# Optimization experiments

Hardware: AMD Instinct MI355X
Metric: run time of the kernel (lower is better)

Reference implementation:

```python
import jax, jax.numpy as jnp
import numpy as np

B, L, D, I = 64, 196, 2048, 512

def setup_inputs() -> dict:
    key = jax.random.key(0)
    ks = jax.random.split(key, 8)
    s_f = 1.0 / np.sqrt(D)
    s_h = 1.0 / np.sqrt(I)
    s_a = 1.0 / np.sqrt(I)
    return {
        "feature_vectors": jax.random.normal(ks[0], (B, L, D), dtype=jnp.float32),
        "hidden_state": jax.random.normal(ks[1], (B, I), dtype=jnp.float32),
        "W_f": jax.random.uniform(ks[2], (D, I), jnp.float32, -s_f, s_f),
        "b_f": jax.random.uniform(ks[3], (I,), jnp.float32, -s_f, s_f),
        "W_h": jax.random.uniform(ks[4], (I, I), jnp.float32, -s_h, s_h),
        "b_h": jax.random.uniform(ks[5], (I,), jnp.float32, -s_h, s_h),
        "W_a": jax.random.uniform(ks[6], (I, D), jnp.float32, -s_a, s_a),
        "b_a": jax.random.uniform(ks[7], (D,), jnp.float32, -s_a, s_a),
    }

def reference(feature_vectors, hidden_state, W_f, b_f, W_h, b_h, W_a, b_a):
    # fv: [B,L,D], hidden: [B,I]
    fv_shaped = jnp.einsum('bld,di->bli', feature_vectors, W_f) + b_f      # [B,L,I]
    hs_shaped = hidden_state @ W_h + b_h                                   # [B,I]
    e = jnp.einsum('bli,id->bld', fv_shaped + hs_shaped[:, None, :], W_a) + b_a  # [B,L,D]
    alpha = jax.nn.softmax(e, axis=1)                                      # softmax over L locations
    z = jnp.sum(alpha * feature_vectors, axis=1)                           # [B,D] (vectorized loop)
    return (z, alpha)
```

## Files before the change

### kernel.cpp

```cpp
#include <hip/hip_runtime.h>

#define B_ 64
#define L_ 196
#define D_ 2048
#define I_ 512
#define M_ (B_*L_)

typedef __attribute__((ext_vector_type(8))) short bf16x8;
typedef __attribute__((ext_vector_type(4))) float f32x4;
typedef unsigned short u16;

__device__ __forceinline__ u16 f2bf(float x){
  unsigned u = __float_as_uint(x);
  u += 0x7fffu + ((u >> 16) & 1u);
  return (u16)(u >> 16);
}

__device__ __forceinline__ void gld16(const void* g, void* l){
  __builtin_amdgcn_global_load_lds(
      (const __attribute__((address_space(1))) void*)g,
      (__attribute__((address_space(3))) void*)l, 16, 0, 0);
}

__global__ void cvt_bf16_kernel(const float* __restrict__ in, u16* __restrict__ out, int n4){
  int i = blockIdx.x*blockDim.x + threadIdx.x;
  int stride = gridDim.x*blockDim.x;
  for (; i < n4; i += stride){
    float4 v = ((const float4*)in)[i];
    ushort4 o;
    o.x = f2bf(v.x); o.y = f2bf(v.y); o.z = f2bf(v.z); o.w = f2bf(v.w);
    ((ushort4*)out)[i] = o;
  }
}

__global__ void transpose_cvt_kernel(const float* __restrict__ in, u16* __restrict__ out, int R, int C){
  __shared__ float tile[32][33];
  int c0 = blockIdx.x*32, r0 = blockIdx.y*32;
  int tx = threadIdx.x, ty = threadIdx.y;
  for (int i=0;i<32;i+=8)
    tile[ty+i][tx] = in[(size_t)(r0+ty+i)*C + c0 + tx];
  __syncthreads();
  for (int i=0;i<32;i+=8)
    out[(size_t)(c0+ty+i)*R + r0 + tx] = f2bf(tile[tx][ty+i]);
}

__global__ void hs_kernel(const float* __restrict__ hidden, const float* __restrict__ Wh,
                          const float* __restrict__ bh, float* __restrict__ hs){
  int n = blockIdx.x*blockDim.x + threadIdx.x;
  int b = blockIdx.y;
  const float* hrow = hidden + b*I_;
  float a0=0.f,a1=0.f,a2=0.f,a3=0.f;
  for (int k=0;k<I_;k+=4){
    a0 = fmaf(hrow[k+0], Wh[(size_t)(k+0)*I_ + n], a0);
    a1 = fmaf(hrow[k+1], Wh[(size_t)(k+1)*I_ + n], a1);
    a2 = fmaf(hrow[k+2], Wh[(size_t)(k+2)*I_ + n], a2);
    a3 = fmaf(hrow[k+3], Wh[(size_t)(k+3)*I_ + n], a3);
  }
  hs[b*I_ + n] = bh[n] + ((a0+a1)+(a2+a3));
}

__launch_bounds__(256)
__global__ void gemm128_kernel(const u16* __restrict__ A,
                               const u16* __restrict__ Bt,
                               int K, int N, int mode,
                               const float* __restrict__ bias,
                               const float* __restrict__ hs,
                               u16* __restrict__ outb,
                               float* __restrict__ outf)
{
  __shared__ __align__(16) u16 Als[128*32];
  __shared__ __align__(16) u16 Bls[128*32];

  const int tid  = threadIdx.x;
  const int lane = tid & 63;
  const int wave = tid >> 6;
  const int m0 = blockIdx.y * 128;
  const int n0 = blockIdx.x * 128;

  const int wrow = (wave & 1) * 64;
  const int wcol = (wave >> 1) * 64;
  const int q  = lane >> 4;
  const int mr = lane & 15;

  const int j0 = wave * 2;
  const int r0i = j0*16     + (lane>>2);
  const int r1i = (j0+1)*16 + (lane>>2);
  const int kc0 = (lane&3) ^ ((r0i>>2)&3);
  const int kc1 = (lane&3) ^ ((r1i>>2)&3);
  const u16* Ag0 = A  + (size_t)(m0 + r0i)*K + kc0*8;
  const u16* Ag1 = A  + (size_t)(m0 + r1i)*K + kc1*8;
  const u16* Bg0 = Bt + (size_t)(n0 + r0i)*K + kc0*8;
  const u16* Bg1 = Bt + (size_t)(n0 + r1i)*K + kc1*8;
  u16* Al0 = Als + (size_t)j0*512;
  u16* Al1 = Als + (size_t)(j0+1)*512;
  u16* Bl0 = Bls + (size_t)j0*512;
  u16* Bl1 = Bls + (size_t)(j0+1)*512;

  int aoff[4], boff[4];
  #pragma unroll
  for (int t=0;t<4;t++){
    int R = wrow + t*16 + mr;
    aoff[t] = (R*4 + (q ^ ((R>>2)&3)))*8;
    int C = wcol + t*16 + mr;
    boff[t] = (C*4 + (q ^ ((C>>2)&3)))*8;
  }

  f32x4 acc[4][4];
  #pragma unroll
  for (int i=0;i<4;i++)
    #pragma unroll
    for (int j=0;j<4;j++) acc[i][j] = (f32x4){0.f,0.f,0.f,0.f};

  for (int k0 = 0; k0 < K; k0 += 32){
    __syncthreads();
    gld16(Ag0 + k0, Al0);
    gld16(Ag1 + k0, Al1);
    gld16(Bg0 + k0, Bl0);
    gld16(Bg1 + k0, Bl1);
    __syncthreads();
    bf16x8 af[4], bg[4];
    #pragma unroll
    for (int t=0;t<4;t++){
      af[t] = *(const bf16x8*)(Als + aoff[t]);
      bg[t] = *(const bf16x8*)(Bls + boff[t]);
    }
    #pragma unroll
    for (int i=0;i<4;i++)
      #pragma unroll
      for (int j=0;j<4;j++)
        acc[i][j] = __builtin_amdgcn_mfma_f32_16x16x32_bf16(af[i], bg[j], acc[i][j], 0,0,0);
  }

  #pragma unroll
  for (int i=0;i<4;i++){
    #pragma unroll
    for (int j=0;j<4;j++){
      int gcol = n0 + wcol + j*16 + mr;
      float bcol = bias[gcol];
      #pragma unroll
      for (int r=0;r<4;r++){
        int grow = m0 + wrow + i*16 + q*4 + r;
        float v = acc[i][j][r] + bcol;
        if (mode == 0){
          int batch = grow / L_;
          outb[(size_t)grow*N + gcol] = f2bf(v + hs[batch*I_ + gcol]);
        } else {
          outf[(size_t)grow*N + gcol] = v;
        }
      }
    }
  }
}

__global__ void softmax_z_kernel(const float* __restrict__ fv, float* __restrict__ out){
  int d = blockIdx.x*blockDim.x + threadIdx.x;
  int b = blockIdx.y;
  float* e = out + (size_t)B_*D_ + (size_t)b*L_*D_ + d;
  const float* f = fv + (size_t)b*L_*D_ + d;
  float m = -3.4e38f, s = 0.f;
  for (int l=0;l<L_;++l){
    float x = e[(size_t)l*D_];
    float nm = fmaxf(m, x);
    s = s*__expf(m-nm) + __expf(x-nm);
    m = nm;
  }
  float inv = 1.f/s;
  float z = 0.f;
  for (int l=0;l<L_;++l){
    float x = e[(size_t)l*D_];
    float a = __expf(x-m)*inv;
    e[(size_t)l*D_] = a;
    z = fmaf(a, f[(size_t)l*D_], z);
  }
  out[(size_t)b*D_ + d] = z;
}

extern "C" void kernel_launch(void* const* d_in, const int* in_sizes, int n_in,
                              void* d_out, int out_size, void* d_ws, size_t ws_size,
                              hipStream_t stream){
  (void)in_sizes; (void)n_in; (void)out_size; (void)ws_size;
  const float* fv     = (const float*)d_in[0];
  const float* hidden = (const float*)d_in[1];
  const float* W_f    = (const float*)d_in[2];
  const float* b_f    = (const float*)d_in[3];
  const float* W_h    = (const float*)d_in[4];
  const float* b_h    = (const float*)d_in[5];
  const float* W_a    = (const float*)d_in[6];
  const float* b_a    = (const float*)d_in[7];
  float* out = (float*)d_out;

  char* ws = (char*)d_ws;
  u16*   fv_bf = (u16*)ws;
  u16*   t_bf  = (u16*)(ws + 51380224);
  u16*   WfT   = (u16*)(ws + 64225280);
  u16*   WaT   = (u16*)(ws + 66322432);
  float* hsbuf = (float*)(ws + 68419584);

  cvt_bf16_kernel<<<4096, 256, 0, stream>>>(fv, fv_bf, (B_*L_*D_)/4);
  transpose_cvt_kernel<<<dim3(I_/32, D_/32), dim3(32,8), 0, stream>>>(W_f, WfT, D_, I_);
  transpose_cvt_kernel<<<dim3(D_/32, I_/32), dim3(32,8), 0, stream>>>(W_a, WaT, I_, D_);
  hs_kernel<<<dim3(I_/256, B_), 256, 0, stream>>>(hidden, W_h, b_h, hsbuf);

  gemm128_kernel<<<dim3(I_/128, M_/128), 256, 0, stream>>>(fv_bf, WfT, D_, I_, 0, b_f, hsbuf, t_bf, nullptr);
  gemm128_kernel<<<dim3(D_/128, M_/128), 256, 0, stream>>>(t_bf, WaT, I_, D_, 1, b_a, nullptr, nullptr, out + B_*D_);

  softmax_z_kernel<<<dim3(D_/256, B_), 256, 0, stream>>>(fv, out);
}
```

Before: 389.8 us.

## Template GEMM with BK=64 tiles, narrower first GEMM, and parallel softmax over L

The GEMM becomes a template with compile-time K, N and mode and a K tile of 64 instead of 32, which halves the number of barrier pairs per K. The first GEMM uses 128x64 tiles so it launches twice as many blocks for the small N=512. The softmax kernel splits the 196 locations across four waves and keeps values in registers, so e is read once instead of twice and more blocks run; the cost is shared-memory reductions and a higher register count.

```diff
diff --git a/kernel.cpp b/kernel.cpp
--- a/kernel.cpp
+++ b/kernel.cpp
@@ -59,120 +59,148 @@
   hs[b*I_ + n] = bh[n] + ((a0+a1)+(a2+a3));
 }
 
+template<int BN, int K, int MODE, int NLD>
 __launch_bounds__(256)
-__global__ void gemm128_kernel(const u16* __restrict__ A,
-                               const u16* __restrict__ Bt,
-                               int K, int N, int mode,
-                               const float* __restrict__ bias,
-                               const float* __restrict__ hs,
-                               u16* __restrict__ outb,
-                               float* __restrict__ outf)
+__global__ void gemm_kernel(const u16* __restrict__ A, const u16* __restrict__ Bt,
+                            const float* __restrict__ bias, const float* __restrict__ hs,
+                            u16* __restrict__ outb, float* __restrict__ outf)
 {
-  __shared__ __align__(16) u16 Als[128*32];
-  __shared__ __align__(16) u16 Bls[128*32];
-
-  const int tid  = threadIdx.x;
-  const int lane = tid & 63;
-  const int wave = tid >> 6;
-  const int m0 = blockIdx.y * 128;
-  const int n0 = blockIdx.x * 128;
-
+  constexpr int BM = 128, BK = 64;
+  constexpr int NF = BN/32;
+  constexpr int AW = 4;
+  constexpr int BW = BN/32;
+
+  __shared__ __align__(16) u16 Als[BM*BK];
+  __shared__ __align__(16) u16 Bls[BN*BK];
+
+  const int tid = threadIdx.x, lane = tid & 63, wave = tid >> 6;
+  const int m0 = blockIdx.y * BM, n0 = blockIdx.x * BN;
+  const int q = lane >> 4, mr = lane & 15;
   const int wrow = (wave & 1) * 64;
-  const int wcol = (wave >> 1) * 64;
-  const int q  = lane >> 4;
-  const int mr = lane & 15;
-
-  const int j0 = wave * 2;
-  const int r0i = j0*16     + (lane>>2);
-  const int r1i = (j0+1)*16 + (lane>>2);
-  const int kc0 = (lane&3) ^ ((r0i>>2)&3);
-  const int kc1 = (lane&3) ^ ((r1i>>2)&3);
-  const u16* Ag0 = A  + (size_t)(m0 + r0i)*K + kc0*8;
-  const u16* Ag1 = A  + (size_t)(m0 + r1i)*K + kc1*8;
-  const u16* Bg0 = Bt + (size_t)(n0 + r0i)*K + kc0*8;
-  const u16* Bg1 = Bt + (size_t)(n0 + r1i)*K + kc1*8;
-  u16* Al0 = Als + (size_t)j0*512;
-  u16* Al1 = Als + (size_t)(j0+1)*512;
-  u16* Bl0 = Bls + (size_t)j0*512;
-  u16* Bl1 = Bls + (size_t)(j0+1)*512;
-
-  int aoff[4], boff[4];
-  #pragma unroll
-  for (int t=0;t<4;t++){
-    int R = wrow + t*16 + mr;
-    aoff[t] = (R*4 + (q ^ ((R>>2)&3)))*8;
-    int C = wcol + t*16 + mr;
-    boff[t] = (C*4 + (q ^ ((C>>2)&3)))*8;
-  }
-
-  f32x4 acc[4][4];
+  const int wcol = (wave >> 1) * (BN/2);
+
+  const int lrow = lane >> 3;
+  const int kc   = (lane & 7) ^ lrow;
+
+  const u16* Ag[AW]; u16* Al[AW];
+  #pragma unroll
+  for (int u=0; u<AW; ++u){
+    int j = wave*AW + u;
+    Ag[u] = A + (size_t)(m0 + j*8 + lrow)*K + kc*8;
+    Al[u] = Als + j*512;
+  }
+  const u16* Bg[BW]; u16* Bl[BW];
+  #pragma unroll
+  for (int u=0; u<BW; ++u){
+    int j = wave*BW + u;
+    Bg[u] = Bt + (size_t)(n0 + j*8 + lrow)*K + kc*8;
+    Bl[u] = Bls + j*512;
+  }
+
+  int aoff[4][2], boff[NF][2];
   #pragma unroll
   for (int i=0;i<4;i++)
     #pragma unroll
-    for (int j=0;j<4;j++) acc[i][j] = (f32x4){0.f,0.f,0.f,0.f};
-
-  for (int k0 = 0; k0 < K; k0 += 32){
+    for (int s=0;s<2;s++){
+      int R = wrow + i*16 + mr;
+      aoff[i][s] = R*64 + (((s*4+q) ^ (mr&7))*8);
+    }
+  #pragma unroll
+  for (int j=0;j<NF;j++)
+    #pragma unroll
+    for (int s=0;s<2;s++){
+      int C = wcol + j*16 + mr;
+      boff[j][s] = C*64 + (((s*4+q) ^ (mr&7))*8);
+    }
+
+  f32x4 acc[4][NF];
+  #pragma unroll
+  for (int i=0;i<4;i++)
+    #pragma unroll
+    for (int j=0;j<NF;j++) acc[i][j] = (f32x4){0.f,0.f,0.f,0.f};
+
+  for (int k0=0; k0<K; k0+=BK){
     __syncthreads();
-    gld16(Ag0 + k0, Al0);
-    gld16(Ag1 + k0, Al1);
-    gld16(Bg0 + k0, Bl0);
-    gld16(Bg1 + k0, Bl1);
+    #pragma unroll
+    for (int u=0;u<AW;++u) gld16(Ag[u] + k0, Al[u]);
+    #pragma unroll
+    for (int u=0;u<BW;++u) gld16(Bg[u] + k0, Bl[u]);
     __syncthreads();
-    bf16x8 af[4], bg[4];
-    #pragma unroll
-    for (int t=0;t<4;t++){
-      af[t] = *(const bf16x8*)(Als + aoff[t]);
-      bg[t] = *(const bf16x8*)(Bls + boff[t]);
-    }
-    #pragma unroll
-    for (int i=0;i<4;i++)
-      #pragma unroll
-      for (int j=0;j<4;j++)
-        acc[i][j] = __builtin_amdgcn_mfma_f32_16x16x32_bf16(af[i], bg[j], acc[i][j], 0,0,0);
+    #pragma unroll
+    for (int s=0;s<2;s++){
+      bf16x8 af[4], bg[NF];
+      #pragma unroll
+      for (int i=0;i<4;i++) af[i] = *(const bf16x8*)(Als + aoff[i][s]);
+      #pragma unroll
+      for (int j=0;j<NF;j++) bg[j] = *(const bf16x8*)(Bls + boff[j][s]);
+      #pragma unroll
+      for (int i=0;i<4;i++)
+        #pragma unroll
+        for (int j=0;j<NF;j++)
+          acc[i][j] = __builtin_amdgcn_mfma_f32_16x16x32_bf16(af[i], bg[j], acc[i][j], 0,0,0);
+    }
   }
 
   #pragma unroll
   for (int i=0;i<4;i++){
     #pragma unroll
-    for (int j=0;j<4;j++){
+    for (int j=0;j<NF;j++){
       int gcol = n0 + wcol + j*16 + mr;
       float bcol = bias[gcol];
       #pragma unroll
       for (int r=0;r<4;r++){
         int grow = m0 + wrow + i*16 + q*4 + r;
         float v = acc[i][j][r] + bcol;
-        if (mode == 0){
+        if (MODE == 0){
           int batch = grow / L_;
-          outb[(size_t)grow*N + gcol] = f2bf(v + hs[batch*I_ + gcol]);
+          outb[(size_t)grow*NLD + gcol] = f2bf(v + hs[batch*I_ + gcol]);
         } else {
-          outf[(size_t)grow*N + gcol] = v;
+          outf[(size_t)grow*NLD + gcol] = v;
         }
       }
     }
   }
 }
 
+__launch_bounds__(256)
 __global__ void softmax_z_kernel(const float* __restrict__ fv, float* __restrict__ out){
-  int d = blockIdx.x*blockDim.x + threadIdx.x;
-  int b = blockIdx.y;
+  __shared__ float red[4][64];
+  const int dl = threadIdx.x & 63, g = threadIdx.x >> 6;
+  const int d = blockIdx.x*64 + dl, b = blockIdx.y;
   float* e = out + (size_t)B_*D_ + (size_t)b*L_*D_ + d;
   const float* f = fv + (size_t)b*L_*D_ + d;
-  float m = -3.4e38f, s = 0.f;
-  for (int l=0;l<L_;++l){
-    float x = e[(size_t)l*D_];
-    float nm = fmaxf(m, x);
-    s = s*__expf(m-nm) + __expf(x-nm);
-    m = nm;
-  }
-  float inv = 1.f/s;
-  float z = 0.f;
-  for (int l=0;l<L_;++l){
-    float x = e[(size_t)l*D_];
-    float a = __expf(x-m)*inv;
-    e[(size_t)l*D_] = a;
-    z = fmaf(a, f[(size_t)l*D_], z);
-  }
-  out[(size_t)b*D_ + d] = z;
+
+  float ev[49];
+  float m = -3.4e38f;
+  #pragma unroll
+  for (int j=0;j<49;j++){
+    ev[j] = e[(size_t)(g*49+j)*D_];
+    m = fmaxf(m, ev[j]);
+  }
+  red[g][dl] = m;
+  __syncthreads();
+  m = fmaxf(fmaxf(red[0][dl],red[1][dl]), fmaxf(red[2][dl],red[3][dl]));
+  __syncthreads();
+
+  float s = 0.f;
+  #pragma unroll
+  for (int j=0;j<49;j++){ ev[j] = __expf(ev[j]-m); s += ev[j]; }
+  red[g][dl] = s;
+  __syncthreads();
+  s = (red[0][dl]+red[1][dl]) + (red[2][dl]+red[3][dl]);
+  __syncthreads();
+
+  float inv = 1.f/s, z = 0.f;
+  #pragma unroll
+  for (int j=0;j<49;j++){
+    float a = ev[j]*inv;
+    e[(size_t)(g*49+j)*D_] = a;
+    z = fmaf(a, f[(size_t)(g*49+j)*D_], z);
+  }
+  red[g][dl] = z;
+  __syncthreads();
+  if (g==0)
+    out[(size_t)b*D_ + dl + blockIdx.x*64] = (red[0][dl]+red[1][dl]) + (red[2][dl]+red[3][dl]);
 }
 
 extern "C" void kernel_launch(void* const* d_in, const int* in_sizes, int n_in,
@@ -201,8 +229,8 @@
   transpose_cvt_kernel<<<dim3(D_/32, I_/32), dim3(32,8), 0, stream>>>(W_a, WaT, I_, D_);
   hs_kernel<<<dim3(I_/256, B_), 256, 0, stream>>>(hidden, W_h, b_h, hsbuf);
 
-  gemm128_kernel<<<dim3(I_/128, M_/128), 256, 0, stream>>>(fv_bf, WfT, D_, I_, 0, b_f, hsbuf, t_bf, nullptr);
-  gemm128_kernel<<<dim3(D_/128, M_/128), 256, 0, stream>>>(t_bf, WaT, I_, D_, 1, b_a, nullptr, nullptr, out + B_*D_);
-
-  softmax_z_kernel<<<dim3(D_/256, B_), 256, 0, stream>>>(fv, out);
-}
+  gemm_kernel<64, D_, 0, I_><<<dim3(I_/64, M_/128), 256, 0, stream>>>(fv_bf, WfT, b_f, hsbuf, t_bf, nullptr);
+  gemm_kernel<128, I_, 1, D_><<<dim3(D_/128, M_/128), 256, 0, stream>>>(t_bf, WaT, b_a, nullptr, nullptr, out + B_*D_);
+
+  softmax_z_kernel<<<dim3(D_/64, B_), 256, 0, stream>>>(fv, out);
+}
```

Result: faster. 372.3 us (-4.5%).
